# Kernel optimization log

Hardware: AMD Instinct MI355X
Metric: run time of the kernel (lower is better)

## Reference

```python
import jax, jax.numpy as jnp
import numpy as np
import math

W = 64  # window_size == chunk_size == 64


def _windows(x, w):
    """x: [b, t, ...] -> [b, nb, 2w, ...]: for block j, concat(block j-1, block j).
    Block -1 is zero padding; its validity is handled by the attention mask."""
    b, t = x.shape[0], x.shape[1]
    nb = t // w
    pad = [(0, 0), (w, 0)] + [(0, 0)] * (x.ndim - 2)
    xp = jnp.pad(x, pad)                                   # [b, t+w, ...]
    xb = xp.reshape((b, nb + 1, w) + x.shape[2:])          # [b, nb+1, w, ...]
    return jnp.concatenate([xb[:, :-1], xb[:, 1:]], axis=2)  # [b, nb, 2w, ...]


def setup_inputs() -> dict:
    key = jax.random.key(0)
    k1, k2, k3 = jax.random.split(key, 3)
    b, t, h, d = 4, 4096, 16, 64
    return {
        "q": jax.random.normal(k1, (b, t, h, d), dtype=jnp.float32),
        "k": jax.random.normal(k2, (b, t, h, d), dtype=jnp.float32),
        "v": jax.random.normal(k3, (b, t, h, d), dtype=jnp.float32),
        "attn_mask": jnp.ones((b, t), dtype=jnp.int32),
    }


def reference(q, k, v, attn_mask):
    b, t, h, d = q.shape
    nb = t // W
    scale = 1.0 / math.sqrt(d)

    qb = q.reshape(b, nb, W, h, d)
    kw = _windows(k, W)                         # [b, nb, 2W, h, d]
    vw = _windows(v, W)                         # [b, nb, 2W, h, d]
    mw = _windows(attn_mask.astype(bool), W)    # [b, nb, 2W]

    # query local index i attends to key local index m iff 0 <= (i+W-m) < W
    i = jnp.arange(W)[:, None]
    m = jnp.arange(2 * W)[None, :]
    diff = i + W - m
    band = (diff >= 0) & (diff < W)             # [W, 2W]

    valid = band[None, None] & mw[:, :, None, :]          # [b, nb, W, 2W]

    scores = jnp.einsum('bnqhd,bnkhd->bnhqk', qb, kw) * scale  # [b,nb,h,W,2W]
    scores = jnp.where(valid[:, :, None], scores, jnp.float32(-1e9))
    attn = jax.nn.softmax(scores, axis=-1)
    attn = attn * valid[:, :, None].astype(attn.dtype)

    qm = attn_mask.astype(q.dtype).reshape(b, nb, W)      # query validity
    attn = attn * qm[:, :, None, :, None]

    out = jnp.einsum('bnhqk,bnkhd->bnqhd', attn, vw)      # [b,nb,W,h,d]
    out = out * qm[:, :, :, None, None]
    return out.reshape(b, t, h, d)
```

## Files before the change

kernel.cpp:

```cpp
#include <hip/hip_runtime.h>
#include <hip/hip_bf16.h>


#define TT 4096
#define HH 16
#define DD 64
#define WW 64
#define NBLK (TT / WW)

typedef __attribute__((ext_vector_type(8))) short bf16x8;
typedef __attribute__((ext_vector_type(4))) float f32x4;

static __device__ __forceinline__ ushort f2bf(float x) {
    return __builtin_bit_cast(unsigned short, __float2bfloat16(x));
}
static __device__ __forceinline__ uint pack2(float a, float b) {
    return (uint)f2bf(a) | ((uint)f2bf(b) << 16);
}

__global__ __launch_bounds__(256, 5)
void lca_fwd(const float* __restrict__ q, const float* __restrict__ k,
             const float* __restrict__ v, const int* __restrict__ am,
             float* __restrict__ out)
{
    const int jb = ((blockIdx.x & 7) << 3) | (blockIdx.x >> 3);
    const int hi = blockIdx.y;
    const int bi = blockIdx.z;

    __shared__ ushort sKP[8192];
    __shared__ ushort sVt[8192];

    const int tid  = threadIdx.x;
    const int wv   = tid >> 6, lane = tid & 63;
    const int quad = lane >> 4, l15 = lane & 15;

    const size_t rowstride = (size_t)HH * DD;
    const size_t qbase = ((size_t)(bi * TT + jb * WW) * HH + hi) * DD;
    const long  kstart = (long)jb * WW - WW;

    const int* amb = am + (size_t)bi * TT;
    long t0 = kstart + lane;
    bool kv0 = (t0 >= 0) && (amb[t0] != 0);
    bool qv  = (amb[jb * WW + lane] != 0);
    unsigned long long kvm_lo = __ballot(kv0);
    unsigned long long qvm    = __ballot(qv);

    float4 fk[8], fv[8], fq[4];
    if (jb > 0) {
        #pragma unroll
        for (int p = 0; p < 8; ++p) {
            int idx = p * 256 + tid;
            int row = idx >> 4, c4 = (idx & 15) * 4;
            fk[p] = *(const float4*)(k + ((size_t)(bi * TT + kstart + row) * HH + hi) * DD + c4);
        }
        #pragma unroll
        for (int p = 0; p < 8; ++p) {
            int idx = p * 256 + tid;
            int row = idx >> 4, c4 = (idx & 15) * 4;
            fv[p] = *(const float4*)(v + ((size_t)(bi * TT + kstart + row) * HH + hi) * DD + c4);
        }
    } else {
        #pragma unroll
        for (int p = 0; p < 8; ++p) {
            float4 z = make_float4(0.f, 0.f, 0.f, 0.f);
            if (p >= 4) {
                int idx = p * 256 + tid;
                int row = idx >> 4, c4 = (idx & 15) * 4;
                z = *(const float4*)(k + ((size_t)(bi * TT + (row - 64)) * HH + hi) * DD + c4);
            }
            fk[p] = z;
        }
        #pragma unroll
        for (int p = 0; p < 8; ++p) {
            float4 z = make_float4(0.f, 0.f, 0.f, 0.f);
            if (p >= 4) {
                int idx = p * 256 + tid;
                int row = idx >> 4, c4 = (idx & 15) * 4;
                z = *(const float4*)(v + ((size_t)(bi * TT + (row - 64)) * HH + hi) * DD + c4);
            }
            fv[p] = z;
        }
    }
    {
        const float* qrow = q + qbase + (size_t)(16 * wv + l15) * rowstride;
        fq[0] = *(const float4*)(qrow + quad * 8);
        fq[1] = *(const float4*)(qrow + quad * 8 + 4);
        fq[2] = *(const float4*)(qrow + 32 + quad * 8);
        fq[3] = *(const float4*)(qrow + 32 + quad * 8 + 4);
    }

    #pragma unroll
    for (int p = 0; p < 8; ++p) {
        int idx = p * 256 + tid;
        int row = idx >> 4, c4 = (idx & 15) * 4;
        uint2 w; w.x = pack2(fk[p].x, fk[p].y); w.y = pack2(fk[p].z, fk[p].w);
        *(uint2*)(&sKP[row * 64 + (((c4 >> 3) ^ (row & 7)) << 3) + (c4 & 7)]) = w;
    }
    #pragma unroll
    for (int p = 0; p < 8; ++p) {
        int idx = p * 256 + tid;
        int row = idx >> 4, c4 = (idx & 15) * 4;
        int u = row >> 3, k7 = row & 7;
        sVt[(c4 + 0) * 128 + ((u ^ ((c4 + 0) & 15)) << 3) + k7] = f2bf(fv[p].x);
        sVt[(c4 + 1) * 128 + ((u ^ ((c4 + 1) & 15)) << 3) + k7] = f2bf(fv[p].y);
        sVt[(c4 + 2) * 128 + ((u ^ ((c4 + 2) & 15)) << 3) + k7] = f2bf(fv[p].z);
        sVt[(c4 + 3) * 128 + ((u ^ ((c4 + 3) & 15)) << 3) + k7] = f2bf(fv[p].w);
    }
    union { bf16x8 v8; uint u[4]; } A0, A1;
    A0.u[0] = pack2(fq[0].x, fq[0].y); A0.u[1] = pack2(fq[0].z, fq[0].w);
    A0.u[2] = pack2(fq[1].x, fq[1].y); A0.u[3] = pack2(fq[1].z, fq[1].w);
    A1.u[0] = pack2(fq[2].x, fq[2].y); A1.u[1] = pack2(fq[2].z, fq[2].w);
    A1.u[2] = pack2(fq[3].x, fq[3].y); A1.u[3] = pack2(fq[3].z, fq[3].w);
    __syncthreads();

    const int r0 = 16 * wv + 4 * quad;
    const int r7 = l15 & 7;

    f32x4 acc[8];
    #pragma unroll
    for (int kt = 0; kt < 8; ++kt) {
        f32x4 a = {0.f, 0.f, 0.f, 0.f};
        const ushort* kr = &sKP[(16 * kt + l15) * 64];
        bf16x8 b0 = *(const bf16x8*)(kr + ((quad ^ r7) << 3));
        bf16x8 b1 = *(const bf16x8*)(kr + (((4 + quad) ^ r7) << 3));
        a = __builtin_amdgcn_mfma_f32_16x16x32_bf16(A0.v8, b0, a, 0, 0, 0);
        a = __builtin_amdgcn_mfma_f32_16x16x32_bf16(A1.v8, b1, a, 0, 0, 0);
        acc[kt] = a;
    }
    __syncthreads();

    const float NEG = -1.0e9f;
    float rmax[4] = {NEG, NEG, NEG, NEG};
    #pragma unroll
    for (int kt = 0; kt < 8; ++kt) {
        int c = 16 * kt + l15;
        unsigned long long km = (kt < 4) ? kvm_lo : qvm;
        int kvc = (int)((km >> (c & 63)) & 1ull);
        #pragma unroll
        for (int reg = 0; reg < 4; ++reg) {
            int r = r0 + reg;
            bool valid = (c > r) && (c <= r + WW) && kvc;
            float s = valid ? acc[kt][reg] : NEG;
            acc[kt][reg] = s;
            rmax[reg] = fmaxf(rmax[reg], s);
        }
    }
    #pragma unroll
    for (int reg = 0; reg < 4; ++reg) {
        #pragma unroll
        for (int m = 1; m <= 8; m <<= 1)
            rmax[reg] = fmaxf(rmax[reg], __shfl_xor(rmax[reg], m, 64));
    }

    const float CEXP = 0.125f * 1.44269504088896f;
    const int l7 = l15 & 7, h3 = l15 >> 3;
    float rsum[4] = {0.f, 0.f, 0.f, 0.f};
    #pragma unroll
    for (int kt = 0; kt < 8; ++kt) {
        int cu = 2 * kt + h3;
        #pragma unroll
        for (int reg = 0; reg < 4; ++reg) {
            float s = acc[kt][reg];
            float pex = (s > -1.0e8f) ? exp2f((s - rmax[reg]) * CEXP) : 0.f;
            rsum[reg] += pex;
            int r = r0 + reg;
            sKP[r * 128 + ((cu ^ (4 * quad + reg)) << 3) + l7] = f2bf(pex);
        }
    }
    float rden[4];
    #pragma unroll
    for (int reg = 0; reg < 4; ++reg) {
        #pragma unroll
        for (int m = 1; m <= 8; m <<= 1)
            rsum[reg] += __shfl_xor(rsum[reg], m, 64);
        rden[reg] = (rsum[reg] > 0.f ? 1.f / rsum[reg] : 0.f)
                    * (float)((qvm >> (r0 + reg)) & 1ull);
    }

    bf16x8 ap[4];
    const ushort* pr = &sKP[(16 * wv + l15) * 128];
    #pragma unroll
    for (int kc = 0; kc < 4; ++kc)
        ap[kc] = *(const bf16x8*)(pr + (((4 * kc + quad) ^ l15) << 3));

    #pragma unroll
    for (int nt = 0; nt < 4; ++nt) {
        f32x4 a = {0.f, 0.f, 0.f, 0.f};
        const ushort* vr = &sVt[(16 * nt + l15) * 128];
        #pragma unroll
        for (int kc = 0; kc < 4; ++kc) {
            bf16x8 bv = *(const bf16x8*)(vr + (((4 * kc + quad) ^ l15) << 3));
            a = __builtin_amdgcn_mfma_f32_16x16x32_bf16(ap[kc], bv, a, 0, 0, 0);
        }
        #pragma unroll
        for (int reg = 0; reg < 4; ++reg)
            out[qbase + (size_t)(r0 + reg) * rowstride + 16 * nt + l15]
                = a[reg] * rden[reg];
    }
}

extern "C" void kernel_launch(void* const* d_in, const int* in_sizes, int n_in,
                              void* d_out, int out_size, void* d_ws, size_t ws_size,
                              hipStream_t stream) {
    const float* q  = (const float*)d_in[0];
    const float* k  = (const float*)d_in[1];
    const float* v  = (const float*)d_in[2];
    const int*   am = (const int*)d_in[3];
    float* out = (float*)d_out;

    const int b = in_sizes[3] / TT;
    dim3 grid(NBLK, HH, b);
    dim3 block(256);
    lca_fwd<<<grid, block, 0, stream>>>(q, k, v, am, out);
}
```

Measured before the change: 229.6 us.

## Process eight consecutive windows per block with double-buffered K/V reuse

Each workgroup now iterates over 8 consecutive 64-row blocks for a head. The previous block's K/V stays in a two-slot shared-memory ring, so each K/V chunk is read from global memory once instead of twice. The next block's K, V and Q are prefetched into registers while the current block computes. P is written into the now-free K slot in two halves to fit the smaller shared buffers. The grid shrinks 8x and occupancy bounds drop, which reduces parallelism available for latency hiding.

```diff
diff --git a/kernel.cpp b/kernel.cpp
--- a/kernel.cpp
+++ b/kernel.cpp
@@ -7,6 +7,8 @@
 #define DD 64
 #define WW 64
 #define NBLK (TT / WW)
+#define NBJ 8
+#define NGRP (NBLK / NBJ)
 
 typedef __attribute__((ext_vector_type(8))) short bf16x8;
 typedef __attribute__((ext_vector_type(4))) float f32x4;
@@ -18,184 +20,241 @@
     return (uint)f2bf(a) | ((uint)f2bf(b) << 16);
 }
 
-__global__ __launch_bounds__(256, 5)
+__global__ __launch_bounds__(256, 2)
 void lca_fwd(const float* __restrict__ q, const float* __restrict__ k,
              const float* __restrict__ v, const int* __restrict__ am,
              float* __restrict__ out)
 {
-    const int jb = ((blockIdx.x & 7) << 3) | (blockIdx.x >> 3);
-    const int hi = blockIdx.y;
-    const int bi = blockIdx.z;
-
-    __shared__ ushort sKP[8192];
-    __shared__ ushort sVt[8192];
+    const int grp = blockIdx.x;
+    const int hi  = blockIdx.y;
+    const int bi  = blockIdx.z;
+    const int jb0 = grp * NBJ;
+
+    __shared__ ushort sK[2][4096];
+    __shared__ ushort sV[2][4096];
 
     const int tid  = threadIdx.x;
     const int wv   = tid >> 6, lane = tid & 63;
     const int quad = lane >> 4, l15 = lane & 15;
+    const int r0   = 16 * wv + 4 * quad;
 
     const size_t rowstride = (size_t)HH * DD;
-    const size_t qbase = ((size_t)(bi * TT + jb * WW) * HH + hi) * DD;
-    const long  kstart = (long)jb * WW - WW;
-
+    const size_t tbase = ((size_t)bi * TT * HH + hi) * DD;
     const int* amb = am + (size_t)bi * TT;
-    long t0 = kstart + lane;
-    bool kv0 = (t0 >= 0) && (amb[t0] != 0);
-    bool qv  = (amb[jb * WW + lane] != 0);
-    unsigned long long kvm_lo = __ballot(kv0);
-    unsigned long long qvm    = __ballot(qv);
-
-    float4 fk[8], fv[8], fq[4];
-    if (jb > 0) {
-        #pragma unroll
-        for (int p = 0; p < 8; ++p) {
-            int idx = p * 256 + tid;
-            int row = idx >> 4, c4 = (idx & 15) * 4;
-            fk[p] = *(const float4*)(k + ((size_t)(bi * TT + kstart + row) * HH + hi) * DD + c4);
-        }
-        #pragma unroll
-        for (int p = 0; p < 8; ++p) {
-            int idx = p * 256 + tid;
-            int row = idx >> 4, c4 = (idx & 15) * 4;
-            fv[p] = *(const float4*)(v + ((size_t)(bi * TT + kstart + row) * HH + hi) * DD + c4);
-        }
-    } else {
-        #pragma unroll
-        for (int p = 0; p < 8; ++p) {
-            float4 z = make_float4(0.f, 0.f, 0.f, 0.f);
-            if (p >= 4) {
-                int idx = p * 256 + tid;
-                int row = idx >> 4, c4 = (idx & 15) * 4;
-                z = *(const float4*)(k + ((size_t)(bi * TT + (row - 64)) * HH + hi) * DD + c4);
-            }
-            fk[p] = z;
-        }
-        #pragma unroll
-        for (int p = 0; p < 8; ++p) {
-            float4 z = make_float4(0.f, 0.f, 0.f, 0.f);
-            if (p >= 4) {
-                int idx = p * 256 + tid;
-                int row = idx >> 4, c4 = (idx & 15) * 4;
-                z = *(const float4*)(v + ((size_t)(bi * TT + (row - 64)) * HH + hi) * DD + c4);
-            }
-            fv[p] = z;
-        }
+
+    const int srow = tid >> 4;
+    const int sc4  = (tid & 15) * 4;
+
+    auto kload = [&](float4* dst, int m) {
+        #pragma unroll
+        for (int p = 0; p < 4; ++p) {
+            int row = p * 16 + srow;
+            dst[p] = *(const float4*)(k + tbase + (size_t)(64 * m + row) * rowstride + sc4);
+        }
+    };
+    auto vload = [&](float4* dst, int m) {
+        #pragma unroll
+        for (int p = 0; p < 4; ++p) {
+            int row = p * 16 + srow;
+            dst[p] = *(const float4*)(v + tbase + (size_t)(64 * m + row) * rowstride + sc4);
+        }
+    };
+    auto qload = [&](float4* dst, int j) {
+        const float* qrow = q + tbase + (size_t)(64 * j + 16 * wv + l15) * rowstride;
+        dst[0] = *(const float4*)(qrow + quad * 8);
+        dst[1] = *(const float4*)(qrow + quad * 8 + 4);
+        dst[2] = *(const float4*)(qrow + 32 + quad * 8);
+        dst[3] = *(const float4*)(qrow + 32 + quad * 8 + 4);
+    };
+    auto kstore = [&](ushort* buf, const float4* src) {
+        #pragma unroll
+        for (int p = 0; p < 4; ++p) {
+            int row = p * 16 + srow;
+            uint2 w; w.x = pack2(src[p].x, src[p].y); w.y = pack2(src[p].z, src[p].w);
+            *(uint2*)(&buf[row * 64 + ((((sc4 >> 3) ^ (row & 7)) & 7) << 3) + (sc4 & 7)]) = w;
+        }
+    };
+    auto vstore = [&](ushort* buf, const float4* src) {
+        #pragma unroll
+        for (int p = 0; p < 4; ++p) {
+            int row = p * 16 + srow;
+            int u = row >> 3, k7 = row & 7;
+            float vals[4] = {src[p].x, src[p].y, src[p].z, src[p].w};
+            #pragma unroll
+            for (int jj = 0; jj < 4; ++jj) {
+                int d = sc4 + jj;
+                int fd = ((d >> 2) ^ d) & 7;
+                buf[d * 64 + (((u ^ fd) & 7) << 3) + k7] = f2bf(vals[jj]);
+            }
+        }
+    };
+
+    {
+        float4 a[4], b[4];
+        if (jb0 > 0) {
+            kload(a, jb0 - 1); vload(b, jb0 - 1);
+            kstore(sK[0], a);  vstore(sV[0], b);
+        } else {
+            #pragma unroll
+            for (int p = 0; p < 4; ++p) {
+                *(uint2*)(&sK[0][(p * 256 + tid) * 4]) = make_uint2(0u, 0u);
+                *(uint2*)(&sV[0][(p * 256 + tid) * 4]) = make_uint2(0u, 0u);
+            }
+        }
+        kload(a, jb0); vload(b, jb0);
+        kstore(sK[1], a); vstore(sV[1], b);
     }
-    {
-        const float* qrow = q + qbase + (size_t)(16 * wv + l15) * rowstride;
-        fq[0] = *(const float4*)(qrow + quad * 8);
-        fq[1] = *(const float4*)(qrow + quad * 8 + 4);
-        fq[2] = *(const float4*)(qrow + 32 + quad * 8);
-        fq[3] = *(const float4*)(qrow + 32 + quad * 8 + 4);
-    }
-
-    #pragma unroll
-    for (int p = 0; p < 8; ++p) {
-        int idx = p * 256 + tid;
-        int row = idx >> 4, c4 = (idx & 15) * 4;
-        uint2 w; w.x = pack2(fk[p].x, fk[p].y); w.y = pack2(fk[p].z, fk[p].w);
-        *(uint2*)(&sKP[row * 64 + (((c4 >> 3) ^ (row & 7)) << 3) + (c4 & 7)]) = w;
-    }
-    #pragma unroll
-    for (int p = 0; p < 8; ++p) {
-        int idx = p * 256 + tid;
-        int row = idx >> 4, c4 = (idx & 15) * 4;
-        int u = row >> 3, k7 = row & 7;
-        sVt[(c4 + 0) * 128 + ((u ^ ((c4 + 0) & 15)) << 3) + k7] = f2bf(fv[p].x);
-        sVt[(c4 + 1) * 128 + ((u ^ ((c4 + 1) & 15)) << 3) + k7] = f2bf(fv[p].y);
-        sVt[(c4 + 2) * 128 + ((u ^ ((c4 + 2) & 15)) << 3) + k7] = f2bf(fv[p].z);
-        sVt[(c4 + 3) * 128 + ((u ^ ((c4 + 3) & 15)) << 3) + k7] = f2bf(fv[p].w);
-    }
-    union { bf16x8 v8; uint u[4]; } A0, A1;
-    A0.u[0] = pack2(fq[0].x, fq[0].y); A0.u[1] = pack2(fq[0].z, fq[0].w);
-    A0.u[2] = pack2(fq[1].x, fq[1].y); A0.u[3] = pack2(fq[1].z, fq[1].w);
-    A1.u[0] = pack2(fq[2].x, fq[2].y); A1.u[1] = pack2(fq[2].z, fq[2].w);
-    A1.u[2] = pack2(fq[3].x, fq[3].y); A1.u[3] = pack2(fq[3].z, fq[3].w);
+    float4 fqc[4];
+    qload(fqc, jb0);
+    unsigned long long qvm_prev = 0;
+    if (jb0 > 0) qvm_prev = __ballot(amb[(jb0 - 1) * 64 + lane] != 0);
     __syncthreads();
 
-    const int r0 = 16 * wv + 4 * quad;
-    const int r7 = l15 & 7;
-
-    f32x4 acc[8];
-    #pragma unroll
-    for (int kt = 0; kt < 8; ++kt) {
-        f32x4 a = {0.f, 0.f, 0.f, 0.f};
-        const ushort* kr = &sKP[(16 * kt + l15) * 64];
-        bf16x8 b0 = *(const bf16x8*)(kr + ((quad ^ r7) << 3));
-        bf16x8 b1 = *(const bf16x8*)(kr + (((4 + quad) ^ r7) << 3));
-        a = __builtin_amdgcn_mfma_f32_16x16x32_bf16(A0.v8, b0, a, 0, 0, 0);
-        a = __builtin_amdgcn_mfma_f32_16x16x32_bf16(A1.v8, b1, a, 0, 0, 0);
-        acc[kt] = a;
-    }
-    __syncthreads();
-
+    const int swl = l15 & 7;
+    const int fdl = ((l15 >> 2) ^ l15) & 7;
     const float NEG = -1.0e9f;
-    float rmax[4] = {NEG, NEG, NEG, NEG};
-    #pragma unroll
-    for (int kt = 0; kt < 8; ++kt) {
-        int c = 16 * kt + l15;
-        unsigned long long km = (kt < 4) ? kvm_lo : qvm;
-        int kvc = (int)((km >> (c & 63)) & 1ull);
+    const float CEXP = 0.125f * 1.44269504088896f;
+
+    for (int bj = 0; bj < NBJ; ++bj) {
+        const int j  = jb0 + bj;
+        const int pb = bj & 1;
+        ushort* kP = sK[pb];
+        ushort* kC = sK[pb ^ 1];
+        ushort* vP = sV[pb];
+        ushort* vC = sV[pb ^ 1];
+
+        unsigned long long qvm = __ballot(amb[j * 64 + lane] != 0);
+        unsigned long long kvm_lo = qvm_prev;
+        qvm_prev = qvm;
+
+        float4 nk[4], nv[4], fqn[4];
+        if (bj < NBJ - 1) { kload(nk, j + 1); vload(nv, j + 1); qload(fqn, j + 1); }
+
+        union { bf16x8 v8; uint u[4]; } A0, A1;
+        A0.u[0] = pack2(fqc[0].x, fqc[0].y); A0.u[1] = pack2(fqc[0].z, fqc[0].w);
+        A0.u[2] = pack2(fqc[1].x, fqc[1].y); A0.u[3] = pack2(fqc[1].z, fqc[1].w);
+        A1.u[0] = pack2(fqc[2].x, fqc[2].y); A1.u[1] = pack2(fqc[2].z, fqc[2].w);
+        A1.u[2] = pack2(fqc[3].x, fqc[3].y); A1.u[3] = pack2(fqc[3].z, fqc[3].w);
+
+        f32x4 acc[8];
+        #pragma unroll
+        for (int kt = 0; kt < 8; ++kt) {
+            const ushort* kr = (kt < 4 ? kP : kC) + (16 * (kt & 3) + l15) * 64;
+            bf16x8 b0 = *(const bf16x8*)(kr + (((quad    ) ^ swl) << 3));
+            bf16x8 b1 = *(const bf16x8*)(kr + (((4 + quad) ^ swl) << 3));
+            f32x4 a = {0.f, 0.f, 0.f, 0.f};
+            a = __builtin_amdgcn_mfma_f32_16x16x32_bf16(A0.v8, b0, a, 0, 0, 0);
+            a = __builtin_amdgcn_mfma_f32_16x16x32_bf16(A1.v8, b1, a, 0, 0, 0);
+            acc[kt] = a;
+        }
+        __syncthreads();
+
+        float rmax[4] = {NEG, NEG, NEG, NEG};
+        #pragma unroll
+        for (int kt = 0; kt < 8; ++kt) {
+            int c = 16 * kt + l15;
+            unsigned long long km = (kt < 4) ? kvm_lo : qvm;
+            int kvc = (int)((km >> (c & 63)) & 1ull);
+            #pragma unroll
+            for (int reg = 0; reg < 4; ++reg) {
+                int r = r0 + reg;
+                bool valid = (c > r) && (c <= r + WW) && kvc;
+                float s = valid ? acc[kt][reg] : NEG;
+                acc[kt][reg] = s;
+                rmax[reg] = fmaxf(rmax[reg], s);
+            }
+        }
+        #pragma unroll
+        for (int reg = 0; reg < 4; ++reg)
+            #pragma unroll
+            for (int m = 1; m <= 8; m <<= 1)
+                rmax[reg] = fmaxf(rmax[reg], __shfl_xor(rmax[reg], m, 64));
+
+        float rsum[4] = {0.f, 0.f, 0.f, 0.f};
+        #pragma unroll
+        for (int kt = 0; kt < 8; ++kt)
+            #pragma unroll
+            for (int reg = 0; reg < 4; ++reg) {
+                float s = acc[kt][reg];
+                float pex = (s > -1.0e8f) ? exp2f((s - rmax[reg]) * CEXP) : 0.f;
+                rsum[reg] += pex;
+                acc[kt][reg] = pex;
+            }
+
+        #pragma unroll
+        for (int kt = 0; kt < 4; ++kt) {
+            int un = 2 * kt + (l15 >> 3), of = l15 & 7;
+            #pragma unroll
+            for (int reg = 0; reg < 4; ++reg) {
+                int r = r0 + reg;
+                kP[r * 64 + (((un ^ ((r ^ (r >> 3)) & 7)) & 7) << 3) + of] = f2bf(acc[kt][reg]);
+            }
+        }
+        float rden[4];
         #pragma unroll
         for (int reg = 0; reg < 4; ++reg) {
-            int r = r0 + reg;
-            bool valid = (c > r) && (c <= r + WW) && kvc;
-            float s = valid ? acc[kt][reg] : NEG;
-            acc[kt][reg] = s;
-            rmax[reg] = fmaxf(rmax[reg], s);
-        }
-    }
-    #pragma unroll
-    for (int reg = 0; reg < 4; ++reg) {
-        #pragma unroll
-        for (int m = 1; m <= 8; m <<= 1)
-            rmax[reg] = fmaxf(rmax[reg], __shfl_xor(rmax[reg], m, 64));
-    }
-
-    const float CEXP = 0.125f * 1.44269504088896f;
-    const int l7 = l15 & 7, h3 = l15 >> 3;
-    float rsum[4] = {0.f, 0.f, 0.f, 0.f};
-    #pragma unroll
-    for (int kt = 0; kt < 8; ++kt) {
-        int cu = 2 * kt + h3;
-        #pragma unroll
-        for (int reg = 0; reg < 4; ++reg) {
-            float s = acc[kt][reg];
-            float pex = (s > -1.0e8f) ? exp2f((s - rmax[reg]) * CEXP) : 0.f;
-            rsum[reg] += pex;
-            int r = r0 + reg;
-            sKP[r * 128 + ((cu ^ (4 * quad + reg)) << 3) + l7] = f2bf(pex);
-        }
-    }
-    float rden[4];
-    #pragma unroll
-    for (int reg = 0; reg < 4; ++reg) {
-        #pragma unroll
-        for (int m = 1; m <= 8; m <<= 1)
-            rsum[reg] += __shfl_xor(rsum[reg], m, 64);
-        rden[reg] = (rsum[reg] > 0.f ? 1.f / rsum[reg] : 0.f)
-                    * (float)((qvm >> (r0 + reg)) & 1ull);
-    }
-
-    bf16x8 ap[4];
-    const ushort* pr = &sKP[(16 * wv + l15) * 128];
-    #pragma unroll
-    for (int kc = 0; kc < 4; ++kc)
-        ap[kc] = *(const bf16x8*)(pr + (((4 * kc + quad) ^ l15) << 3));
-
-    #pragma unroll
-    for (int nt = 0; nt < 4; ++nt) {
-        f32x4 a = {0.f, 0.f, 0.f, 0.f};
-        const ushort* vr = &sVt[(16 * nt + l15) * 128];
-        #pragma unroll
-        for (int kc = 0; kc < 4; ++kc) {
-            bf16x8 bv = *(const bf16x8*)(vr + (((4 * kc + quad) ^ l15) << 3));
-            a = __builtin_amdgcn_mfma_f32_16x16x32_bf16(ap[kc], bv, a, 0, 0, 0);
-        }
-        #pragma unroll
-        for (int reg = 0; reg < 4; ++reg)
-            out[qbase + (size_t)(r0 + reg) * rowstride + 16 * nt + l15]
-                = a[reg] * rden[reg];
+            #pragma unroll
+            for (int m = 1; m <= 8; m <<= 1)
+                rsum[reg] += __shfl_xor(rsum[reg], m, 64);
+            rden[reg] = (rsum[reg] > 0.f ? 1.f / rsum[reg] : 0.f)
+                        * (float)((qvm >> (r0 + reg)) & 1ull);
+        }
+
+        const int prow = 16 * wv + l15;
+        const int psw  = (prow ^ (prow >> 3)) & 7;
+        bf16x8 ap0 = *(const bf16x8*)(&kP[prow * 64 + (((quad    ) ^ psw) << 3)]);
+        bf16x8 ap1 = *(const bf16x8*)(&kP[prow * 64 + (((4 + quad) ^ psw) << 3)]);
+        f32x4 po[4];
+        #pragma unroll
+        for (int nt = 0; nt < 4; ++nt) {
+            int fd = fdl ^ (4 * (nt & 1));
+            const ushort* vr = &vP[(16 * nt + l15) * 64];
+            bf16x8 bv0 = *(const bf16x8*)(vr + ((((quad    ) ^ fd) & 7) << 3));
+            bf16x8 bv1 = *(const bf16x8*)(vr + ((((4 + quad) ^ fd) & 7) << 3));
+            f32x4 a = {0.f, 0.f, 0.f, 0.f};
+            a = __builtin_amdgcn_mfma_f32_16x16x32_bf16(ap0, bv0, a, 0, 0, 0);
+            a = __builtin_amdgcn_mfma_f32_16x16x32_bf16(ap1, bv1, a, 0, 0, 0);
+            po[nt] = a;
+        }
+
+        #pragma unroll
+        for (int kt = 4; kt < 8; ++kt) {
+            int un = 2 * (kt - 4) + (l15 >> 3), of = l15 & 7;
+            #pragma unroll
+            for (int reg = 0; reg < 4; ++reg) {
+                int r = r0 + reg;
+                kP[r * 64 + (((un ^ ((r ^ (r >> 3)) & 7)) & 7) << 3) + of] = f2bf(acc[kt][reg]);
+            }
+        }
+        ap0 = *(const bf16x8*)(&kP[prow * 64 + (((quad    ) ^ psw) << 3)]);
+        ap1 = *(const bf16x8*)(&kP[prow * 64 + (((4 + quad) ^ psw) << 3)]);
+        #pragma unroll
+        for (int nt = 0; nt < 4; ++nt) {
+            int fd = fdl ^ (4 * (nt & 1));
+            const ushort* vr = &vC[(16 * nt + l15) * 64];
+            bf16x8 bv0 = *(const bf16x8*)(vr + ((((quad    ) ^ fd) & 7) << 3));
+            bf16x8 bv1 = *(const bf16x8*)(vr + ((((4 + quad) ^ fd) & 7) << 3));
+            f32x4 a = po[nt];
+            a = __builtin_amdgcn_mfma_f32_16x16x32_bf16(ap0, bv0, a, 0, 0, 0);
+            a = __builtin_amdgcn_mfma_f32_16x16x32_bf16(ap1, bv1, a, 0, 0, 0);
+            po[nt] = a;
+        }
+
+        const size_t obase = tbase + (size_t)(j * 64) * rowstride;
+        #pragma unroll
+        for (int nt = 0; nt < 4; ++nt)
+            #pragma unroll
+            for (int reg = 0; reg < 4; ++reg)
+                out[obase + (size_t)(r0 + reg) * rowstride + 16 * nt + l15]
+                    = po[nt][reg] * rden[reg];
+
+        if (bj < NBJ - 1) {
+            __syncthreads();
+            kstore(kP, nk);
+            vstore(vP, nv);
+            fqc[0] = fqn[0]; fqc[1] = fqn[1]; fqc[2] = fqn[2]; fqc[3] = fqn[3];
+            __syncthreads();
+        }
     }
 }
 
@@ -206,10 +265,10 @@
     const float* k  = (const float*)d_in[1];
     const float* v  = (const float*)d_in[2];
     const int*   am = (const int*)d_in[3];
-    float* out = (float*)d_out;
+    float* outp = (float*)d_out;
 
     const int b = in_sizes[3] / TT;
-    dim3 grid(NBLK, HH, b);
+    dim3 grid(NGRP, HH, b);
     dim3 block(256);
-    lca_fwd<<<grid, block, 0, stream>>>(q, k, v, am, out);
-}
+    lca_fwd<<<grid, block, 0, stream>>>(q, k, v, am, outp);
+}
```

New measurement: 229.3 us. No clear change (-0.1%).
